# Kernel optimization log

Hardware: AMD Instinct MI355X
Metric: run time of the kernel (lower is better)

Reference implementation:

```python
import jax, jax.numpy as jnp
import numpy as np

N, E, G = 50000, 800000, 64
H, C = 4, 64
IN = 260
SPLITS = [7, 4, 6, 4, 8]  # types, levels, interchange, unrolling, tiling


def _glorot(k, shape):
    lim = (6.0 / (shape[0] + shape[-1])) ** 0.5
    return jax.random.uniform(k, shape, jnp.float32, -lim, lim)


def setup_inputs() -> dict:
    key = jax.random.key(0)
    ks = list(jax.random.split(key, 40))
    nk = lambda: ks.pop()
    x = jax.random.normal(nk(), (N, IN), jnp.float32)
    edge_index = jax.random.randint(nk(), (2, E), 0, N)
    batch = ((jnp.arange(N) * G) // N).astype(jnp.int32)  # sorted, every graph non-empty
    input_actions = jnp.stack([jax.random.randint(nk(), (G,), 0, s) for s in SPLITS], 0)
    p = dict(
        W1=_glorot(nk(), (IN, H * C)), a_s1=jax.random.normal(nk(), (H, C)) * 0.1,
        a_d1=jax.random.normal(nk(), (H, C)) * 0.1, b1=jnp.zeros((H * C,)),
        Wl1=_glorot(nk(), (H * C, C)), bl1=jnp.zeros((C,)),
        W2=_glorot(nk(), (C, H * C)), a_s2=jax.random.normal(nk(), (H, C)) * 0.1,
        a_d2=jax.random.normal(nk(), (H, C)) * 0.1, b2=jnp.zeros((H * C,)),
        Wl2=_glorot(nk(), (H * C, C)), bl2=jnp.zeros((C,)),
        Ws=_glorot(nk(), (4 * C, 2 * C)), bs=jnp.zeros((2 * C,)),
        Wsh=_glorot(nk(), (2 * C, C)), bsh=jnp.zeros((C,)),
        Wp1=_glorot(nk(), (C, C)), bp1=jnp.zeros((C,)),
        Wp2=_glorot(nk(), (C, C)), bp2=jnp.zeros((C,)),
        Wp3=_glorot(nk(), (C, sum(SPLITS))), bp3=jnp.zeros((sum(SPLITS),)),
        Wv1=_glorot(nk(), (C, C)), bv1=jnp.zeros((C,)),
        Wv2=_glorot(nk(), (C, C)), bv2=jnp.zeros((C,)),
        Wv3=_glorot(nk(), (C, 1)), bv3=jnp.zeros((1,)),
    )
    return dict(x=x, edge_index=edge_index, batch=batch, input_actions=input_actions, **p)


def gat_conv(x, W, a_src, a_dst, b, src, dst, n):
    h = (x @ W).reshape(n, H, C)                          # [N,H,C]
    es = (h * a_src).sum(-1)                              # [N,H]
    ed = (h * a_dst).sum(-1)
    e = jax.nn.leaky_relu(es[src] + ed[dst], 0.2)          # [Etot,H]
    m = jax.ops.segment_max(e, dst, n)
    ex = jnp.exp(e - m[dst])
    denom = jax.ops.segment_sum(ex, dst, n)
    alpha = ex / denom[dst]                                # edge softmax per dst node
    out = jax.ops.segment_sum(alpha[:, :, None] * h[src], dst, n)
    return out.reshape(n, H * C) + b


def pool(x, batch, g):
    cnt = jax.ops.segment_sum(jnp.ones((x.shape[0],), x.dtype), batch, g)
    mean = jax.ops.segment_sum(x, batch, g) / cnt[:, None]
    mx = jax.ops.segment_max(x, batch, g)
    return jnp.concatenate([mean, mx], -1)


def reference(x, edge_index, batch, input_actions, W1, a_s1, a_d1, b1, Wl1, bl1,
              W2, a_s2, a_d2, b2, Wl2, bl2, Ws, bs, Wsh, bsh,
              Wp1, bp1, Wp2, bp2, Wp3, bp3, Wv1, bv1, Wv2, bv2, Wv3, bv3):
    n = x.shape[0]
    loop = jnp.arange(n)
    src = jnp.concatenate([edge_index[0], loop])  # add self loops (PyG default)
    dst = jnp.concatenate([edge_index[1], loop])
    h = gat_conv(x, W1, a_s1, a_d1, b1, src, dst, n)
    h = jax.nn.selu(h @ Wl1 + bl1)
    x1 = pool(h, batch, G)
    h = gat_conv(h, W2, a_s2, a_d2, b2, src, dst, n)
    h = jax.nn.selu(h @ Wl2 + bl2)
    x2 = pool(h, batch, G)
    g = jnp.concatenate([x1, x2], -1) @ Ws + bs
    g = jax.nn.selu(g @ Wsh + bsh)
    hp = jax.nn.selu(g @ Wp1 + bp1)
    hp = jax.nn.selu(hp @ Wp2 + bp2)
    raw_logits = hp @ Wp3 + bp3
    hv = jax.nn.selu(g @ Wv1 + bv1)
    hv = jax.nn.selu(hv @ Wv2 + bv2)
    value = hv @ Wv3 + bv3                               # [G,1]
    parts = jnp.split(raw_logits, np.cumsum(SPLITS)[:-1].tolist(), axis=1)
    lps, ents = [], []
    for k, lg in enumerate(parts):
        logp = jax.nn.log_softmax(lg, -1)
        lps.append(jnp.take_along_axis(logp, input_actions[k][:, None], 1)[:, 0])
        ents.append(-(jnp.exp(logp) * logp).sum(-1))
    lp, en = jnp.stack(lps), jnp.stack(ents)              # [5,G]
    act = input_actions[0]
    bidx = jnp.arange(G)
    sel = jnp.clip(act - 1, 0, 4)
    lp_sel, en_sel = lp[sel, bidx], en[sel, bidx]
    zero = jnp.zeros_like(lp[0])
    final_lp = lp[0] + jnp.where(act < 3, lp[1], jnp.where(act < 5, lp_sel, jnp.where(act == 5, lp[1] + lp[4], zero)))
    final_en = en[0] + jnp.where(act < 3, en[1], jnp.where(act < 5, en_sel, jnp.where(act == 5, en[1] + en[4], zero)))
    return final_lp, final_en, value
```

## Files before the change

### kernel.cpp

```cpp
#include <hip/hip_runtime.h>
#include <math.h>

static constexpr int G_  = 64;
static constexpr int H_  = 4;
static constexpr int C_  = 64;
static constexpr int IN_ = 260;
static constexpr int HC_ = 256;
static constexpr int PAD_ = 64;
static constexpr int SLOTS_ = 16;

typedef short short8 __attribute__((ext_vector_type(8)));
typedef float f32x4 __attribute__((ext_vector_type(4)));

__device__ __forceinline__ float lrelu02(float x) { return x >= 0.f ? x : 0.2f * x; }
__device__ __forceinline__ float selu_f(float x) {
  const float sc = 1.0507009873554805f, al = 1.6732632423543772f;
  return x > 0.f ? sc * x : sc * al * expm1f(x);
}
__device__ __forceinline__ float bf2f(unsigned short u) {
  return __uint_as_float(((unsigned int)u) << 16);
}
__device__ __forceinline__ unsigned short f2bf(float f) {
  unsigned int u = __float_as_uint(f);
  u = (u + 0x7FFFu + ((u >> 16) & 1u)) >> 16;
  return (unsigned short)u;
}
__device__ __forceinline__ int lower_bound_i(const int* b, int n, int val) {
  int lo = 0, hi = n;
  while (lo < hi) {
    int mid = (lo + hi) >> 1;
    if (b[mid] < val) lo = mid + 1; else hi = mid;
  }
  return lo;
}

__global__ __launch_bounds__(256) void k_prep(const float* __restrict__ x, ushort4* __restrict__ xb,
                                              const float* __restrict__ W1, const float* __restrict__ W2,
                                              const float* __restrict__ Wl1, const float* __restrict__ Wl2,
                                              unsigned short* __restrict__ wout, int* __restrict__ cur,
                                              int* __restrict__ pcnt1, int* __restrict__ pcnt2,
                                              int n, int Mpad) {
  int idx = blockIdx.x * 256 + threadIdx.x;
  int castTotal = Mpad * 72;
  if (idx < castTotal) {
    int r = idx / 72, c4 = (idx - r * 72) * 4;
    ushort4 o = make_ushort4(0, 0, 0, 0);
    if (r < n && c4 < IN_) {
      float4 v = *(const float4*)&x[(size_t)r * IN_ + c4];
      o = make_ushort4(f2bf(v.x), f2bf(v.y), f2bf(v.z), f2bf(v.w));
    }
    xb[idx] = o;
    return;
  }
  idx -= castTotal;
  if (idx < 122880) {
    const float* W;
    int Kreal, KS, N, local;
    if (idx < 73728)       { W = W1;  Kreal = 260; KS = 9; N = 256; local = idx; }
    else if (idx < 90112)  { W = W2;  Kreal = 64;  KS = 2; N = 256; local = idx - 73728; }
    else if (idx < 106496) { W = Wl1; Kreal = 256; KS = 8; N = 64;  local = idx - 90112; }
    else                   { W = Wl2; Kreal = 256; KS = 8; N = 64;  local = idx - 106496; }
    int i = local & 7;
    int l = (local >> 3) & 63;
    int nb = (local >> 9) & 3;
    int ks = (local >> 11) % KS;
    int g = (local >> 11) / KS;
    int k = ks * 32 + ((l >> 4) << 3) + i;
    int n2 = g * 64 + nb * 16 + (l & 15);
    wout[idx] = (k < Kreal) ? f2bf(W[(size_t)k * N + n2]) : (unsigned short)0;
    return;
  }
  idx -= 122880;
  if (idx < n) { cur[idx] = 0; return; }
  idx -= n;
  if (idx < 1024) { pcnt1[idx] = 0; return; }
  idx -= 1024;
  if (idx < 1024) pcnt2[idx] = 0;
}

__global__ __launch_bounds__(256) void k_scatter(const int* __restrict__ src, const int* __restrict__ dst,
                                                 int* __restrict__ cur, unsigned short* __restrict__ csr, int E) {
  int e = blockIdx.x * 256 + threadIdx.x;
  if (e < E) {
    int d = dst[e];
    int pos = atomicAdd(&cur[d], 1);
    if (pos < PAD_) csr[(d << 6) + pos] = (unsigned short)src[e];
  }
}

template <int KS>
__global__ __launch_bounds__(256) void k_mgemm(const unsigned short* __restrict__ A,
                                               const unsigned short* __restrict__ Bp,
                                               unsigned short* __restrict__ C,
                                               int Kpad, int N) {
  extern __shared__ char smem[];
  unsigned short* lds = (unsigned short*)smem;
  int tid = threadIdx.x;
  int l = tid & 63;
  int w = tid >> 6;
  int g = blockIdx.y;
  {
    const float4* s = (const float4*)(Bp + (size_t)g * KS * 2048);
    float4* d = (float4*)lds;
    #pragma unroll
    for (int t = 0; t < KS; t++) d[t * 256 + tid] = s[t * 256 + tid];
  }
  __syncthreads();
  int rm = blockIdx.x * 256 + w * 64;
  const unsigned short* arow[4];
  #pragma unroll
  for (int mi = 0; mi < 4; mi++)
    arow[mi] = A + (size_t)(rm + mi * 16 + (l & 15)) * Kpad + ((l >> 4) << 3);
  f32x4 acc[4][4] = {};
  #pragma unroll
  for (int ks = 0; ks < KS; ks++) {
    short8 a[4], b[4];
    #pragma unroll
    for (int mi = 0; mi < 4; mi++) a[mi] = *(const short8*)(arow[mi] + ks * 32);
    #pragma unroll
    for (int nb = 0; nb < 4; nb++) b[nb] = *(const short8*)(lds + (((ks * 4 + nb) * 64) + l) * 8);
    #pragma unroll
    for (int mi = 0; mi < 4; mi++)
      #pragma unroll
      for (int nb = 0; nb < 4; nb++)
        acc[mi][nb] = __builtin_amdgcn_mfma_f32_16x16x32_bf16(a[mi], b[nb], acc[mi][nb], 0, 0, 0);
  }
  int cr = (l >> 4) * 4;
  int cc = l & 15;
  #pragma unroll
  for (int mi = 0; mi < 4; mi++) {
    #pragma unroll
    for (int nb = 0; nb < 4; nb++) {
      int col = g * 64 + nb * 16 + cc;
      int colp = (col & 63) * 4 + (col >> 6);
      #pragma unroll
      for (int r = 0; r < 4; r++)
        C[(size_t)(rm + mi * 16 + cr + r) * N + colp] = f2bf(acc[mi][nb][r]);
    }
  }
}

__global__ __launch_bounds__(256) void k_esedq(const unsigned short* __restrict__ h, const float* __restrict__ a_s,
                                               const float* __restrict__ a_d, float* __restrict__ esed,
                                               unsigned int* __restrict__ hq, float* __restrict__ scale, int n) {
  int lane = threadIdx.x & 63;
  int node = blockIdx.x * 4 + (threadIdx.x >> 6);
  if (node >= n) return;
  ushort4 u = *(const ushort4*)(h + (size_t)node * HC_ + lane * 4);
  float xv[4] = {bf2f(u.x), bf2f(u.y), bf2f(u.z), bf2f(u.w)};
  float s[H_], d[H_];
  float amax = 0.f;
  #pragma unroll
  for (int hh = 0; hh < H_; hh++) {
    s[hh] = xv[hh] * a_s[hh * C_ + lane];
    d[hh] = xv[hh] * a_d[hh * C_ + lane];
    amax = fmaxf(amax, fabsf(xv[hh]));
  }
  #pragma unroll
  for (int o2 = 32; o2 > 0; o2 >>= 1) {
    #pragma unroll
    for (int hh = 0; hh < H_; hh++) {
      s[hh] += __shfl_xor(s[hh], o2, 64);
      d[hh] += __shfl_xor(d[hh], o2, 64);
    }
    amax = fmaxf(amax, __shfl_xor(amax, o2, 64));
  }
  float sc = fmaxf(amax, 1e-6f) * (1.f / 127.f);
  float inv = 127.f / fmaxf(amax, 1e-6f);
  unsigned int q = 0;
  #pragma unroll
  for (int hh = 0; hh < H_; hh++) {
    int qi = __float2int_rn(xv[hh] * inv);
    qi = min(127, max(-127, qi)) + 128;
    q |= ((unsigned int)qi) << (8 * hh);
  }
  hq[(size_t)node * 64 + lane] = q;
  if (lane == 0) {
    scale[node] = sc;
    #pragma unroll
    for (int hh = 0; hh < H_; hh++) {
      esed[(size_t)node * 8 + hh] = s[hh];
      esed[(size_t)node * 8 + 4 + hh] = d[hh];
    }
  }
}

__global__ __launch_bounds__(256) void k_agg(const unsigned int* __restrict__ hq, const float* __restrict__ scale,
                                             const float* __restrict__ esed, const int* __restrict__ deg,
                                             const unsigned short* __restrict__ csr, const float* __restrict__ bias,
                                             unsigned short* __restrict__ out, int n) {
  __shared__ float4 wlds[4][64];
  __shared__ int slds[4][64];
  int lane = threadIdx.x & 63;
  int wv = threadIdx.x >> 6;
  int node = blockIdx.x * 4 + wv;
  if (node >= n) return;
  int nk = min(deg[node], PAD_);
  int e0 = node << 6;
  const float4 edv = ((const float4*)esed)[(size_t)node * 2 + 1];
  float acc0 = 0.f, acc1 = 0.f, acc2 = 0.f, acc3 = 0.f;
  float den[4] = {0.f, 0.f, 0.f, 0.f};
  float sw[4] = {0.f, 0.f, 0.f, 0.f};
  {
    float4 w4 = make_float4(0.f, 0.f, 0.f, 0.f);
    int sid = 0;
    if (lane < nk) {
      sid = csr[e0 + lane];
      float4 es = ((const float4*)esed)[(size_t)sid * 2];
      float sc = scale[sid];
      float w0 = __expf(lrelu02(es.x + edv.x));
      float w1 = __expf(lrelu02(es.y + edv.y));
      float w2 = __expf(lrelu02(es.z + edv.z));
      float w3 = __expf(lrelu02(es.w + edv.w));
      den[0] += w0; den[1] += w1; den[2] += w2; den[3] += w3;
      w4 = make_float4(w0 * sc, w1 * sc, w2 * sc, w3 * sc);
      sw[0] += w4.x; sw[1] += w4.y; sw[2] += w4.z; sw[3] += w4.w;
    }
    wlds[wv][lane] = w4;
    slds[wv][lane] = sid << 8;
  }
  const char* hqb = (const char*)hq + lane * 4;
#define AGG1(W, Q)                                        \
  acc0 = fmaf(W.x, (float)(Q & 0xffu), acc0);             \
  acc1 = fmaf(W.y, (float)((Q >> 8) & 0xffu), acc1);      \
  acc2 = fmaf(W.z, (float)((Q >> 16) & 0xffu), acc2);     \
  acc3 = fmaf(W.w, (float)(Q >> 24), acc3);
  int j = 0;
  for (; j + 4 <= nk; j += 4) {
    float4 wa = wlds[wv][j], wb = wlds[wv][j + 1], wc = wlds[wv][j + 2], wd = wlds[wv][j + 3];
    int oa = slds[wv][j], ob = slds[wv][j + 1], oc = slds[wv][j + 2], od = slds[wv][j + 3];
    unsigned int qa = *(const unsigned int*)(hqb + oa);
    unsigned int qb = *(const unsigned int*)(hqb + ob);
    unsigned int qc = *(const unsigned int*)(hqb + oc);
    unsigned int qd = *(const unsigned int*)(hqb + od);
    AGG1(wa, qa) AGG1(wb, qb) AGG1(wc, qc) AGG1(wd, qd)
  }
  for (; j < nk; j++) {
    float4 wj = wlds[wv][j];
    unsigned int q = *(const unsigned int*)(hqb + slds[wv][j]);
    AGG1(wj, q)
  }
#undef AGG1
  #pragma unroll
  for (int o2 = 32; o2 > 0; o2 >>= 1) {
    #pragma unroll
    for (int hh = 0; hh < 4; hh++) {
      den[hh] += __shfl_xor(den[hh], o2, 64);
      sw[hh] += __shfl_xor(sw[hh], o2, 64);
    }
  }
  const float4 esv = ((const float4*)esed)[(size_t)node * 2];
  float ssc = scale[node];
  unsigned int qs = hq[(size_t)node * 64 + lane];
  float es0 = __expf(lrelu02(esv.x + edv.x));
  float es1 = __expf(lrelu02(esv.y + edv.y));
  float es2 = __expf(lrelu02(esv.z + edv.z));
  float es3 = __expf(lrelu02(esv.w + edv.w));
  float w0 = es0 * ssc, w1 = es1 * ssc, w2 = es2 * ssc, w3 = es3 * ssc;
  acc0 = fmaf(w0, (float)(qs & 0xffu), acc0);
  acc1 = fmaf(w1, (float)((qs >> 8) & 0xffu), acc1);
  acc2 = fmaf(w2, (float)((qs >> 16) & 0xffu), acc2);
  acc3 = fmaf(w3, (float)(qs >> 24), acc3);
  den[0] += es0; den[1] += es1; den[2] += es2; den[3] += es3;
  sw[0] += w0; sw[1] += w1; sw[2] += w2; sw[3] += w3;
  float r0 = (acc0 - 128.f * sw[0]) / den[0];
  float r1 = (acc1 - 128.f * sw[1]) / den[1];
  float r2 = (acc2 - 128.f * sw[2]) / den[2];
  float r3 = (acc3 - 128.f * sw[3]) / den[3];
  out[(size_t)node * HC_ + 0 * C_ + lane] = f2bf(r0 + bias[0 * C_ + lane]);
  out[(size_t)node * HC_ + 1 * C_ + lane] = f2bf(r1 + bias[1 * C_ + lane]);
  out[(size_t)node * HC_ + 2 * C_ + lane] = f2bf(r2 + bias[2 * C_ + lane]);
  out[(size_t)node * HC_ + 3 * C_ + lane] = f2bf(r3 + bias[3 * C_ + lane]);
}

template <int PHASE2>
__global__ __launch_bounds__(256) void k_fuse(const unsigned short* __restrict__ gout,
                                              const unsigned short* __restrict__ Bl, const float* __restrict__ bl,
                                              const unsigned short* __restrict__ W2p,
                                              const float* __restrict__ as2, const float* __restrict__ ad2,
                                              float* __restrict__ esed, unsigned int* __restrict__ hq,
                                              float* __restrict__ scale,
                                              const int* __restrict__ batch,
                                              float* __restrict__ psum, float* __restrict__ pmax,
                                              int* __restrict__ pcnt, int n) {
  __shared__ unsigned short hs_lds[64 * 64];
  __shared__ float pA_s[4][64], pA_m[4][64], pB_s[4][64], pB_m[4][64];
  __shared__ int meta[4];
  int tid = threadIdx.x;
  int l = tid & 63;
  int w = tid >> 6;
  int bm = blockIdx.x * 64;
  {
    const unsigned short* arow = gout + (size_t)(bm + w * 16 + (l & 15)) * HC_ + ((l >> 4) << 3);
    f32x4 acc[4] = {};
    #pragma unroll
    for (int ks = 0; ks < 8; ks++) {
      short8 a = *(const short8*)(arow + ks * 32);
      #pragma unroll
      for (int nb = 0; nb < 4; nb++) {
        short8 b = *(const short8*)(Bl + (size_t)(ks * 2048 + nb * 512 + l * 8));
        acc[nb] = __builtin_amdgcn_mfma_f32_16x16x32_bf16(a, b, acc[nb], 0, 0, 0);
      }
    }
    #pragma unroll
    for (int nb = 0; nb < 4; nb++) {
      #pragma unroll
      for (int r = 0; r < 4; r++) {
        int row = w * 16 + (l >> 4) * 4 + r;
        int col = nb * 16 + (l & 15);
        float v = selu_f(acc[nb][r] + bl[col]);
        int chunk = (col >> 3) ^ (row & 7);
        hs_lds[row * 64 + chunk * 8 + (col & 7)] = f2bf(v);
      }
    }
  }
  __syncthreads();
  if (PHASE2) {
    f32x4 acc2[16] = {};
    #pragma unroll
    for (int ks2 = 0; ks2 < 2; ks2++) {
      int row = w * 16 + (l & 15);
      int chunk = (ks2 * 4 + (l >> 4)) ^ (row & 7);
      short8 a2 = *(const short8*)(hs_lds + row * 64 + chunk * 8);
      #pragma unroll
      for (int f = 0; f < 16; f++) {
        short8 b2 = *(const short8*)(W2p + (size_t)(((f >> 2) * 2 + ks2) * 2048 + (f & 3) * 512 + l * 8));
        acc2[f] = __builtin_amdgcn_mfma_f32_16x16x32_bf16(a2, b2, acc2[f], 0, 0, 0);
      }
    }
    float s_[4][4] = {}, d_[4][4] = {};
    float am[4] = {0.f, 0.f, 0.f, 0.f};
    #pragma unroll
    for (int f = 0; f < 16; f++) {
      int ch = (f >> 2) * 64 + (f & 3) * 16 + (l & 15);
      float asv = as2[ch], adv = ad2[ch];
      #pragma unroll
      for (int r = 0; r < 4; r++) {
        float v = acc2[f][r];
        s_[r][f >> 2] = fmaf(v, asv, s_[r][f >> 2]);
        d_[r][f >> 2] = fmaf(v, adv, d_[r][f >> 2]);
        am[r] = fmaxf(am[r], fabsf(v));
      }
    }
    #pragma unroll
    for (int off = 1; off < 16; off <<= 1) {
      #pragma unroll
      for (int r = 0; r < 4; r++) {
        #pragma unroll
        for (int g2 = 0; g2 < 4; g2++) {
          s_[r][g2] += __shfl_xor(s_[r][g2], off, 64);
          d_[r][g2] += __shfl_xor(d_[r][g2], off, 64);
        }
        am[r] = fmaxf(am[r], __shfl_xor(am[r], off, 64));
      }
    }
    #pragma unroll
    for (int r = 0; r < 4; r++) {
      int node = bm + w * 16 + (l >> 4) * 4 + r;
      if (node < n) {
        float amax = fmaxf(am[r], 1e-6f);
        float inv = 127.f / amax;
        #pragma unroll
        for (int nb = 0; nb < 4; nb++) {
          unsigned int q = 0;
          #pragma unroll
          for (int g2 = 0; g2 < 4; g2++) {
            int qi = __float2int_rn(acc2[g2 * 4 + nb][r] * inv);
            qi = min(127, max(-127, qi)) + 128;
            q |= ((unsigned int)qi) << (8 * g2);
          }
          hq[(size_t)node * 64 + nb * 16 + (l & 15)] = q;
        }
        int li = l & 15;
        if (li < 4) esed[(size_t)node * 8 + li] = s_[r][li];
        else if (li < 8) esed[(size_t)node * 8 + li] = d_[r][li - 4];
        else if (li == 8) scale[node] = amax * (1.f / 127.f);
      }
    }
  }
  if (tid == 0) {
    int gA = (bm < n) ? batch[bm] : -1;
    int valid = n - bm;
    valid = valid < 0 ? 0 : (valid > 64 ? 64 : valid);
    int split = valid, gB = -1;
    if (gA >= 0) {
      int lb = lower_bound_i(batch, n, gA + 1);
      split = lb - bm;
      if (split > valid) split = valid;
      if (split < valid) gB = batch[bm + split];
    }
    meta[0] = gA; meta[1] = split; meta[2] = gB; meta[3] = valid;
  }
  __syncthreads();
  int gA = meta[0], split = meta[1], gB = meta[2], valid = meta[3];
  if (gA < 0) return;
  {
    int ch = tid & 63, rs = tid >> 6;
    float sA = 0.f, mA = -INFINITY, sB = 0.f, mB = -INFINITY;
    #pragma unroll
    for (int k = 0; k < 16; k++) {
      int r = rs * 16 + k;
      if (r < valid) {
        int chunk = (ch >> 3) ^ (r & 7);
        float v = bf2f(hs_lds[r * 64 + chunk * 8 + (ch & 7)]);
        if (r < split) { sA += v; mA = fmaxf(mA, v); }
        else           { sB += v; mB = fmaxf(mB, v); }
      }
    }
    pA_s[rs][ch] = sA; pA_m[rs][ch] = mA;
    pB_s[rs][ch] = sB; pB_m[rs][ch] = mB;
  }
  __syncthreads();
  if (tid < 64) {
    float s = pA_s[0][tid] + pA_s[1][tid] + pA_s[2][tid] + pA_s[3][tid];
    float m = fmaxf(fmaxf(pA_m[0][tid], pA_m[1][tid]), fmaxf(pA_m[2][tid], pA_m[3][tid]));
    int slotA = (int)blockIdx.x - (lower_bound_i(batch, n, gA) >> 6);
    psum[((size_t)gA * SLOTS_ + slotA) * 64 + tid] = s;
    pmax[((size_t)gA * SLOTS_ + slotA) * 64 + tid] = m;
    if (tid == 0) pcnt[gA * SLOTS_ + slotA] = split;
  } else if (tid < 128 && gB >= 0) {
    int c2 = tid - 64;
    float s = pB_s[0][c2] + pB_s[1][c2] + pB_s[2][c2] + pB_s[3][c2];
    float m = fmaxf(fmaxf(pB_m[0][c2], pB_m[1][c2]), fmaxf(pB_m[2][c2], pB_m[3][c2]));
    psum[((size_t)gB * SLOTS_ + 0) * 64 + c2] = s;
    pmax[((size_t)gB * SLOTS_ + 0) * 64 + c2] = m;
    if (c2 == 0) pcnt[gB * SLOTS_] = valid - split;
  }
}

__global__ __launch_bounds__(128) void k_head(const float* __restrict__ psum1, const float* __restrict__ pmax1,
                                              const int* __restrict__ pcnt1,
                                              const float* __restrict__ psum2, const float* __restrict__ pmax2,
                                              const int* __restrict__ pcnt2, const int* __restrict__ ia,
                                              const float* __restrict__ Ws, const float* __restrict__ bs,
                                              const float* __restrict__ Wsh, const float* __restrict__ bsh,
                                              const float* __restrict__ Wp1, const float* __restrict__ bp1,
                                              const float* __restrict__ Wp2, const float* __restrict__ bp2,
                                              const float* __restrict__ Wp3, const float* __restrict__ bp3,
                                              const float* __restrict__ Wv1, const float* __restrict__ bv1,
                                              const float* __restrict__ Wv2, const float* __restrict__ bv2,
                                              const float* __restrict__ Wv3, const float* __restrict__ bv3,
                                              float* __restrict__ out) {
  int g = blockIdx.x;
  int t = threadIdx.x;
  __shared__ float row[256], t1[128], g2[64], ha[64], hb[64], ha2[64], hb2[64];
  __shared__ float logits[29], lps[5], ens[5];
  {
    const float* PS = (t < 64) ? psum1 : psum2;
    const float* PM = (t < 64) ? pmax1 : pmax2;
    const int* PC = (t < 64) ? pcnt1 : pcnt2;
    int c = t & 63;
    int o = (t < 64) ? 0 : 128;
    float sum = 0.f, mx = -INFINITY;
    int tot = 0;
    #pragma unroll
    for (int s = 0; s < SLOTS_; s++) {
      int c0 = PC[g * SLOTS_ + s];
      if (c0 > 0) {
        sum += PS[((size_t)g * SLOTS_ + s) * 64 + c];
        mx = fmaxf(mx, PM[((size_t)g * SLOTS_ + s) * 64 + c]);
        tot += c0;
      }
    }
    row[o + c] = sum / (float)tot;
    row[o + 64 + c] = mx;
  }
  __syncthreads();
  {
    float a = bs[t];
    for (int k = 0; k < 256; k++) a = fmaf(row[k], Ws[k * 128 + t], a);
    t1[t] = a;
  }
  __syncthreads();
  if (t < 64) {
    float a = bsh[t];
    for (int k = 0; k < 128; k++) a = fmaf(t1[k], Wsh[k * 64 + t], a);
    g2[t] = selu_f(a);
  }
  __syncthreads();
  if (t < 64) {
    float a = bp1[t];
    for (int k = 0; k < 64; k++) a = fmaf(g2[k], Wp1[k * 64 + t], a);
    ha[t] = selu_f(a);
  } else {
    int c = t - 64;
    float a = bv1[c];
    for (int k = 0; k < 64; k++) a = fmaf(g2[k], Wv1[k * 64 + c], a);
    hb[c] = selu_f(a);
  }
  __syncthreads();
  if (t < 64) {
    float a = bp2[t];
    for (int k = 0; k < 64; k++) a = fmaf(ha[k], Wp2[k * 64 + t], a);
    ha2[t] = selu_f(a);
  } else {
    int c = t - 64;
    float a = bv2[c];
    for (int k = 0; k < 64; k++) a = fmaf(hb[k], Wv2[k * 64 + c], a);
    hb2[c] = selu_f(a);
  }
  __syncthreads();
  if (t < 29) {
    float a = bp3[t];
    for (int k = 0; k < 64; k++) a = fmaf(ha2[k], Wp3[k * 29 + t], a);
    logits[t] = a;
  }
  if (t == 127) {
    float a = bv3[0];
    for (int k = 0; k < 64; k++) a = fmaf(hb2[k], Wv3[k], a);
    out[128 + g] = a;
  }
  __syncthreads();
  if (t < 5) {
    const int offs[6] = {0, 7, 11, 17, 21, 29};
    int o0 = offs[t], o1 = offs[t + 1];
    float m = -INFINITY;
    for (int j = o0; j < o1; j++) m = fmaxf(m, logits[j]);
    float Z = 0.f;
    for (int j = o0; j < o1; j++) Z += expf(logits[j] - m);
    float lz = logf(Z);
    int act = ia[t * G_ + g];
    lps[t] = logits[o0 + act] - m - lz;
    float ent = 0.f;
    for (int j = o0; j < o1; j++) {
      float lp_ = logits[j] - m - lz;
      ent -= expf(lp_) * lp_;
    }
    ens[t] = ent;
  }
  __syncthreads();
  if (t == 0) {
    int act = ia[g];
    int sel = min(max(act - 1, 0), 4);
    float flp, fen;
    if (act < 3) { flp = lps[1]; fen = ens[1]; }
    else if (act < 5) { flp = lps[sel]; fen = ens[sel]; }
    else if (act == 5) { flp = lps[1] + lps[4]; fen = ens[1] + ens[4]; }
    else { flp = 0.f; fen = 0.f; }
    out[g] = lps[0] + flp;
    out[G_ + g] = ens[0] + fen;
  }
}

extern "C" void kernel_launch(void* const* d_in, const int* in_sizes, int n_in,
                              void* d_out, int out_size, void* d_ws, size_t ws_size,
                              hipStream_t stream) {
  const float* x = (const float*)d_in[0];
  const int* ei = (const int*)d_in[1];
  const int* batch = (const int*)d_in[2];
  const int* ia = (const int*)d_in[3];
  const float* W1 = (const float*)d_in[4];
  const float* as1 = (const float*)d_in[5];
  const float* ad1 = (const float*)d_in[6];
  const float* b1 = (const float*)d_in[7];
  const float* Wl1 = (const float*)d_in[8];
  const float* bl1 = (const float*)d_in[9];
  const float* W2 = (const float*)d_in[10];
  const float* as2 = (const float*)d_in[11];
  const float* ad2 = (const float*)d_in[12];
  const float* b2 = (const float*)d_in[13];
  const float* Wl2 = (const float*)d_in[14];
  const float* bl2 = (const float*)d_in[15];
  const float* Ws = (const float*)d_in[16];
  const float* bs = (const float*)d_in[17];
  const float* Wsh = (const float*)d_in[18];
  const float* bsh = (const float*)d_in[19];
  const float* Wp1 = (const float*)d_in[20];
  const float* bp1 = (const float*)d_in[21];
  const float* Wp2 = (const float*)d_in[22];
  const float* bp2 = (const float*)d_in[23];
  const float* Wp3 = (const float*)d_in[24];
  const float* bp3 = (const float*)d_in[25];
  const float* Wv1 = (const float*)d_in[26];
  const float* bv1 = (const float*)d_in[27];
  const float* Wv2 = (const float*)d_in[28];
  const float* bv2 = (const float*)d_in[29];
  const float* Wv3 = (const float*)d_in[30];
  const float* bv3 = (const float*)d_in[31];
  float* out = (float*)d_out;

  const int n = in_sizes[0] / IN_;
  const int E = in_sizes[1] / 2;
  const int Mpad = ((n + 255) / 256) * 256;
  const int* src = ei;
  const int* dst = ei + E;

  char* w = (char*)d_ws;
  size_t cur_off = 0;
  auto alloc = [&](size_t bytes) -> char* {
    char* p = w + cur_off;
    cur_off = (cur_off + bytes + 255) & ~(size_t)255;
    return p;
  };
  int* cur = (int*)alloc((size_t)n * 4);
  int* pcnt1 = (int*)alloc((size_t)G_ * SLOTS_ * 4);
  int* pcnt2 = (int*)alloc((size_t)G_ * SLOTS_ * 4);
  unsigned short* csr = (unsigned short*)alloc((size_t)n * PAD_ * 2);
  unsigned short* xb = (unsigned short*)alloc((size_t)Mpad * 288 * 2);
  unsigned short* h = (unsigned short*)alloc((size_t)Mpad * HC_ * 2);
  float* esed = (float*)alloc((size_t)n * 8 * 4);
  float* scale = (float*)alloc((size_t)n * 4);
  unsigned int* hq = (unsigned int*)alloc((size_t)n * 256);
  unsigned short* gout = (unsigned short*)alloc((size_t)Mpad * HC_ * 2);
  unsigned short* Wp = (unsigned short*)alloc((size_t)122880 * 2);
  float* psum1 = (float*)alloc((size_t)G_ * SLOTS_ * 64 * 4);
  float* pmax1 = (float*)alloc((size_t)G_ * SLOTS_ * 64 * 4);
  float* psum2 = (float*)alloc((size_t)G_ * SLOTS_ * 64 * 4);
  float* pmax2 = (float*)alloc((size_t)G_ * SLOTS_ * 64 * 4);
  (void)ws_size;
  (void)n_in;
  (void)out_size;
  unsigned short* W1p = Wp;
  unsigned short* W2p = Wp + 73728;
  unsigned short* Wl1p = Wp + 90112;
  unsigned short* Wl2p = Wp + 106496;

  int prepTotal = Mpad * 72 + 122880 + n + 2048;
  k_prep<<<(prepTotal + 255) / 256, 256, 0, stream>>>(x, (ushort4*)xb, W1, W2, Wl1, Wl2, Wp,
                                                      cur, pcnt1, pcnt2, n, Mpad);
  int eb = (E + 255) / 256;
  k_scatter<<<eb, 256, 0, stream>>>(src, dst, cur, csr, E);

  int gx = Mpad / 256;
  int nwb = (n + 3) / 4;
  int fb = Mpad / 64;
  k_mgemm<9><<<dim3(gx, 4), 256, 9 * 4096, stream>>>(xb, W1p, h, 288, HC_);
  k_esedq<<<nwb, 256, 0, stream>>>(h, as1, ad1, esed, hq, scale, n);
  k_agg<<<nwb, 256, 0, stream>>>(hq, scale, esed, cur, csr, b1, gout, n);
  k_fuse<1><<<fb, 256, 0, stream>>>(gout, Wl1p, bl1, W2p, as2, ad2, esed, hq, scale,
                                    batch, psum1, pmax1, pcnt1, n);
  k_agg<<<nwb, 256, 0, stream>>>(hq, scale, esed, cur, csr, b2, gout, n);
  k_fuse<0><<<fb, 256, 0, stream>>>(gout, Wl2p, bl2, nullptr, nullptr, nullptr, nullptr, nullptr, nullptr,
                                    batch, psum2, pmax2, pcnt2, n);
  k_head<<<G_, 128, 0, stream>>>(psum1, pmax1, pcnt1, psum2, pmax2, pcnt2, ia, Ws, bs, Wsh, bsh,
                                 Wp1, bp1, Wp2, bp2, Wp3, bp3, Wv1, bv1, Wv2, bv2, Wv3, bv3, out);
}
```

Measured before the change: 298.9 us.

## Replace padded per-node edge buckets with exact CSR via count and prefix scan

Builds a compact CSR adjacency instead of the fixed 64-slot padded buckets. It counts in-degrees inside the prep kernel, runs a three-kernel block prefix scan to get offsets, then scatters source ids to exact positions. k_agg now reads offsets. This removes the truncation at 64 neighbours during the build and shrinks csr storage, but adds a memset, three small kernels and an extra atomic pass over all edges. Aggregation still caps each node's neighbour count at 64.

```diff
diff --git a/kernel.cpp b/kernel.cpp
--- a/kernel.cpp
+++ b/kernel.cpp
@@ -37,9 +37,10 @@
 __global__ __launch_bounds__(256) void k_prep(const float* __restrict__ x, ushort4* __restrict__ xb,
                                               const float* __restrict__ W1, const float* __restrict__ W2,
                                               const float* __restrict__ Wl1, const float* __restrict__ Wl2,
-                                              unsigned short* __restrict__ wout, int* __restrict__ cur,
+                                              unsigned short* __restrict__ wout,
                                               int* __restrict__ pcnt1, int* __restrict__ pcnt2,
-                                              int n, int Mpad) {
+                                              const int* __restrict__ dst, int* __restrict__ cnt,
+                                              int n, int Mpad, int E) {
   int idx = blockIdx.x * 256 + threadIdx.x;
   int castTotal = Mpad * 72;
   if (idx < castTotal) {
@@ -71,11 +72,76 @@
     return;
   }
   idx -= 122880;
-  if (idx < n) { cur[idx] = 0; return; }
-  idx -= n;
   if (idx < 1024) { pcnt1[idx] = 0; return; }
   idx -= 1024;
-  if (idx < 1024) pcnt2[idx] = 0;
+  if (idx < 1024) { pcnt2[idx] = 0; return; }
+  idx -= 1024;
+  if (idx < E) atomicAdd(&cnt[dst[idx]], 1);
+}
+
+__global__ __launch_bounds__(256) void k_bsum(const int* __restrict__ cnt, int* __restrict__ bsum, int n) {
+  int b = blockIdx.x, tid = threadIdx.x;
+  int i0 = b * 1024 + tid * 4;
+  int s = 0;
+  #pragma unroll
+  for (int j = 0; j < 4; j++)
+    if (i0 + j < n) s += cnt[i0 + j];
+  #pragma unroll
+  for (int o = 32; o > 0; o >>= 1) s += __shfl_xor(s, o, 64);
+  __shared__ int ws_[4];
+  if ((tid & 63) == 0) ws_[tid >> 6] = s;
+  __syncthreads();
+  if (tid == 0) bsum[b] = ws_[0] + ws_[1] + ws_[2] + ws_[3];
+}
+
+__global__ __launch_bounds__(64) void k_bscan(int* __restrict__ bsum, int nb, int* __restrict__ off,
+                                              int n, int total) {
+  int lane = threadIdx.x;
+  int carry = 0;
+  for (int base = 0; base < nb; base += 64) {
+    int v = (base + lane < nb) ? bsum[base + lane] : 0;
+    int sc = v;
+    #pragma unroll
+    for (int s = 1; s < 64; s <<= 1) {
+      int t = __shfl_up(sc, s, 64);
+      if (lane >= s) sc += t;
+    }
+    if (base + lane < nb) bsum[base + lane] = carry + sc - v;
+    carry += __shfl(sc, 63, 64);
+  }
+  if (lane == 0) off[n] = total;
+}
+
+__global__ __launch_bounds__(256) void k_boff(const int* __restrict__ cnt, const int* __restrict__ bpre,
+                                              int* __restrict__ off, int* __restrict__ cur, int n) {
+  int b = blockIdx.x, tid = threadIdx.x;
+  int lane = tid & 63, w = tid >> 6;
+  int i0 = b * 1024 + tid * 4;
+  int v[4];
+  #pragma unroll
+  for (int j = 0; j < 4; j++) v[j] = (i0 + j < n) ? cnt[i0 + j] : 0;
+  int ts = v[0] + v[1] + v[2] + v[3];
+  int sc = ts;
+  #pragma unroll
+  for (int s = 1; s < 64; s <<= 1) {
+    int t = __shfl_up(sc, s, 64);
+    if (lane >= s) sc += t;
+  }
+  __shared__ int wsum[4], wpre[4];
+  if (lane == 63) wsum[w] = sc;
+  __syncthreads();
+  if (tid == 0) {
+    int a = 0;
+    #pragma unroll
+    for (int k = 0; k < 4; k++) { wpre[k] = a; a += wsum[k]; }
+  }
+  __syncthreads();
+  int excl = bpre[b] + wpre[w] + sc - ts;
+  #pragma unroll
+  for (int j = 0; j < 4; j++) {
+    if (i0 + j < n) { off[i0 + j] = excl; cur[i0 + j] = excl; }
+    excl += v[j];
+  }
 }
 
 __global__ __launch_bounds__(256) void k_scatter(const int* __restrict__ src, const int* __restrict__ dst,
@@ -84,7 +150,7 @@
   if (e < E) {
     int d = dst[e];
     int pos = atomicAdd(&cur[d], 1);
-    if (pos < PAD_) csr[(d << 6) + pos] = (unsigned short)src[e];
+    csr[pos] = (unsigned short)src[e];
   }
 }
 
@@ -186,7 +252,7 @@
 }
 
 __global__ __launch_bounds__(256) void k_agg(const unsigned int* __restrict__ hq, const float* __restrict__ scale,
-                                             const float* __restrict__ esed, const int* __restrict__ deg,
+                                             const float* __restrict__ esed, const int* __restrict__ off,
                                              const unsigned short* __restrict__ csr, const float* __restrict__ bias,
                                              unsigned short* __restrict__ out, int n) {
   __shared__ float4 wlds[4][64];
@@ -195,8 +261,8 @@
   int wv = threadIdx.x >> 6;
   int node = blockIdx.x * 4 + wv;
   if (node >= n) return;
-  int nk = min(deg[node], PAD_);
-  int e0 = node << 6;
+  int e0 = off[node];
+  int nk = min(off[node + 1] - e0, PAD_);
   const float4 edv = ((const float4*)esed)[(size_t)node * 2 + 1];
   float acc0 = 0.f, acc1 = 0.f, acc2 = 0.f, acc3 = 0.f;
   float den[4] = {0.f, 0.f, 0.f, 0.f};
@@ -343,15 +409,15 @@
       }
     }
     #pragma unroll
-    for (int off = 1; off < 16; off <<= 1) {
+    for (int off2 = 1; off2 < 16; off2 <<= 1) {
       #pragma unroll
       for (int r = 0; r < 4; r++) {
         #pragma unroll
         for (int g2 = 0; g2 < 4; g2++) {
-          s_[r][g2] += __shfl_xor(s_[r][g2], off, 64);
-          d_[r][g2] += __shfl_xor(d_[r][g2], off, 64);
+          s_[r][g2] += __shfl_xor(s_[r][g2], off2, 64);
+          d_[r][g2] += __shfl_xor(d_[r][g2], off2, 64);
         }
-        am[r] = fmaxf(am[r], __shfl_xor(am[r], off, 64));
+        am[r] = fmaxf(am[r], __shfl_xor(am[r], off2, 64));
       }
     }
     #pragma unroll
@@ -582,6 +648,7 @@
   const int n = in_sizes[0] / IN_;
   const int E = in_sizes[1] / 2;
   const int Mpad = ((n + 255) / 256) * 256;
+  const int nb = (n + 1023) / 1024;
   const int* src = ei;
   const int* dst = ei + E;
 
@@ -592,10 +659,13 @@
     cur_off = (cur_off + bytes + 255) & ~(size_t)255;
     return p;
   };
+  int* cnt = (int*)alloc((size_t)n * 4);
+  int* off = (int*)alloc((size_t)(n + 1) * 4);
   int* cur = (int*)alloc((size_t)n * 4);
+  int* bsum = (int*)alloc((size_t)(nb + 1) * 4);
   int* pcnt1 = (int*)alloc((size_t)G_ * SLOTS_ * 4);
   int* pcnt2 = (int*)alloc((size_t)G_ * SLOTS_ * 4);
-  unsigned short* csr = (unsigned short*)alloc((size_t)n * PAD_ * 2);
+  unsigned short* csr = (unsigned short*)alloc((size_t)E * 2);
   unsigned short* xb = (unsigned short*)alloc((size_t)Mpad * 288 * 2);
   unsigned short* h = (unsigned short*)alloc((size_t)Mpad * HC_ * 2);
   float* esed = (float*)alloc((size_t)n * 8 * 4);
@@ -615,9 +685,13 @@
   unsigned short* Wl1p = Wp + 90112;
   unsigned short* Wl2p = Wp + 106496;
 
-  int prepTotal = Mpad * 72 + 122880 + n + 2048;
+  hipMemsetAsync(cnt, 0, (size_t)n * 4, stream);
+  int prepTotal = Mpad * 72 + 122880 + 2048 + E;
   k_prep<<<(prepTotal + 255) / 256, 256, 0, stream>>>(x, (ushort4*)xb, W1, W2, Wl1, Wl2, Wp,
-                                                      cur, pcnt1, pcnt2, n, Mpad);
+                                                      pcnt1, pcnt2, dst, cnt, n, Mpad, E);
+  k_bsum<<<nb, 256, 0, stream>>>(cnt, bsum, n);
+  k_bscan<<<1, 64, 0, stream>>>(bsum, nb, off, n, E);
+  k_boff<<<nb, 256, 0, stream>>>(cnt, bsum, off, cur, n);
   int eb = (E + 255) / 256;
   k_scatter<<<eb, 256, 0, stream>>>(src, dst, cur, csr, E);
 
@@ -626,10 +700,10 @@
   int fb = Mpad / 64;
   k_mgemm<9><<<dim3(gx, 4), 256, 9 * 4096, stream>>>(xb, W1p, h, 288, HC_);
   k_esedq<<<nwb, 256, 0, stream>>>(h, as1, ad1, esed, hq, scale, n);
-  k_agg<<<nwb, 256, 0, stream>>>(hq, scale, esed, cur, csr, b1, gout, n);
+  k_agg<<<nwb, 256, 0, stream>>>(hq, scale, esed, off, csr, b1, gout, n);
   k_fuse<1><<<fb, 256, 0, stream>>>(gout, Wl1p, bl1, W2p, as2, ad2, esed, hq, scale,
                                     batch, psum1, pmax1, pcnt1, n);
-  k_agg<<<nwb, 256, 0, stream>>>(hq, scale, esed, cur, csr, b2, gout, n);
+  k_agg<<<nwb, 256, 0, stream>>>(hq, scale, esed, off, csr, b2, gout, n);
   k_fuse<0><<<fb, 256, 0, stream>>>(gout, Wl2p, bl2, nullptr, nullptr, nullptr, nullptr, nullptr, nullptr,
                                     batch, psum2, pmax2, pcnt2, n);
   k_head<<<G_, 128, 0, stream>>>(psum1, pmax1, pcnt1, psum2, pmax2, pcnt2, ia, Ws, bs, Wsh, bsh,
```

Result: slower. 338.9 us (+13.4%).

## Fuse layer-1 GEMM with attention-score and int8 quantization epilogue

Applied to the files above, without the earlier changes.

Replaces the separate bf16 GEMM (which wrote h to global) and the k_esedq pass with one kernel that computes the x@W1 tile via MFMA and directly produces attention scores, per-node scale and quantized features. This removes the h round-trip through global memory and one launch. W1 fragments are now read straight from global/cache instead of staged in LDS, and each block does only 64 rows, which may raise weight traffic. Separately, the CSR neighbour list changes from 16-bit to 32-bit ints written with atomicExch, which fixes truncation for node ids above 65535 but doubles CSR bytes.

```diff
diff --git a/kernel.cpp b/kernel.cpp
--- a/kernel.cpp
+++ b/kernel.cpp
@@ -79,115 +79,89 @@
 }
 
 __global__ __launch_bounds__(256) void k_scatter(const int* __restrict__ src, const int* __restrict__ dst,
-                                                 int* __restrict__ cur, unsigned short* __restrict__ csr, int E) {
+                                                 int* __restrict__ cur, int* __restrict__ csr, int E) {
   int e = blockIdx.x * 256 + threadIdx.x;
   if (e < E) {
     int d = dst[e];
     int pos = atomicAdd(&cur[d], 1);
-    if (pos < PAD_) csr[(d << 6) + pos] = (unsigned short)src[e];
-  }
-}
-
-template <int KS>
-__global__ __launch_bounds__(256) void k_mgemm(const unsigned short* __restrict__ A,
-                                               const unsigned short* __restrict__ Bp,
-                                               unsigned short* __restrict__ C,
-                                               int Kpad, int N) {
-  extern __shared__ char smem[];
-  unsigned short* lds = (unsigned short*)smem;
+    if (pos < PAD_) atomicExch(&csr[(d << 6) + pos], src[e]);
+  }
+}
+
+__global__ __launch_bounds__(256) void k_l1(const unsigned short* __restrict__ xb,
+                                            const unsigned short* __restrict__ W1p,
+                                            const float* __restrict__ as1, const float* __restrict__ ad1,
+                                            float* __restrict__ esed, unsigned int* __restrict__ hq,
+                                            float* __restrict__ scale, int n) {
   int tid = threadIdx.x;
   int l = tid & 63;
   int w = tid >> 6;
-  int g = blockIdx.y;
-  {
-    const float4* s = (const float4*)(Bp + (size_t)g * KS * 2048);
-    float4* d = (float4*)lds;
-    #pragma unroll
-    for (int t = 0; t < KS; t++) d[t * 256 + tid] = s[t * 256 + tid];
-  }
-  __syncthreads();
-  int rm = blockIdx.x * 256 + w * 64;
-  const unsigned short* arow[4];
+  int bm = blockIdx.x * 64;
+  const unsigned short* arow = xb + (size_t)(bm + w * 16 + (l & 15)) * 288 + ((l >> 4) << 3);
+  f32x4 acc2[16] = {};
   #pragma unroll
-  for (int mi = 0; mi < 4; mi++)
-    arow[mi] = A + (size_t)(rm + mi * 16 + (l & 15)) * Kpad + ((l >> 4) << 3);
-  f32x4 acc[4][4] = {};
+  for (int ks = 0; ks < 9; ks++) {
+    short8 a = *(const short8*)(arow + ks * 32);
+    #pragma unroll
+    for (int f = 0; f < 16; f++) {
+      short8 b = *(const short8*)(W1p + (size_t)(((f >> 2) * 9 + ks) * 2048 + (f & 3) * 512 + l * 8));
+      acc2[f] = __builtin_amdgcn_mfma_f32_16x16x32_bf16(a, b, acc2[f], 0, 0, 0);
+    }
+  }
+  float s_[4][4] = {}, d_[4][4] = {};
+  float am[4] = {0.f, 0.f, 0.f, 0.f};
   #pragma unroll
-  for (int ks = 0; ks < KS; ks++) {
-    short8 a[4], b[4];
-    #pragma unroll
-    for (int mi = 0; mi < 4; mi++) a[mi] = *(const short8*)(arow[mi] + ks * 32);
-    #pragma unroll
-    for (int nb = 0; nb < 4; nb++) b[nb] = *(const short8*)(lds + (((ks * 4 + nb) * 64) + l) * 8);
-    #pragma unroll
-    for (int mi = 0; mi < 4; mi++)
+  for (int f = 0; f < 16; f++) {
+    int ch = (f >> 2) * 64 + (f & 3) * 16 + (l & 15);
+    float asv = as1[ch], adv = ad1[ch];
+    #pragma unroll
+    for (int r = 0; r < 4; r++) {
+      float v = acc2[f][r];
+      s_[r][f >> 2] = fmaf(v, asv, s_[r][f >> 2]);
+      d_[r][f >> 2] = fmaf(v, adv, d_[r][f >> 2]);
+      am[r] = fmaxf(am[r], fabsf(v));
+    }
+  }
+  #pragma unroll
+  for (int off2 = 1; off2 < 16; off2 <<= 1) {
+    #pragma unroll
+    for (int r = 0; r < 4; r++) {
       #pragma unroll
-      for (int nb = 0; nb < 4; nb++)
-        acc[mi][nb] = __builtin_amdgcn_mfma_f32_16x16x32_bf16(a[mi], b[nb], acc[mi][nb], 0, 0, 0);
-  }
-  int cr = (l >> 4) * 4;
-  int cc = l & 15;
+      for (int g2 = 0; g2 < 4; g2++) {
+        s_[r][g2] += __shfl_xor(s_[r][g2], off2, 64);
+        d_[r][g2] += __shfl_xor(d_[r][g2], off2, 64);
+      }
+      am[r] = fmaxf(am[r], __shfl_xor(am[r], off2, 64));
+    }
+  }
   #pragma unroll
-  for (int mi = 0; mi < 4; mi++) {
-    #pragma unroll
-    for (int nb = 0; nb < 4; nb++) {
-      int col = g * 64 + nb * 16 + cc;
-      int colp = (col & 63) * 4 + (col >> 6);
+  for (int r = 0; r < 4; r++) {
+    int node = bm + w * 16 + (l >> 4) * 4 + r;
+    if (node < n) {
+      float amax = fmaxf(am[r], 1e-6f);
+      float inv = 127.f / amax;
       #pragma unroll
-      for (int r = 0; r < 4; r++)
-        C[(size_t)(rm + mi * 16 + cr + r) * N + colp] = f2bf(acc[mi][nb][r]);
-    }
-  }
-}
-
-__global__ __launch_bounds__(256) void k_esedq(const unsigned short* __restrict__ h, const float* __restrict__ a_s,
-                                               const float* __restrict__ a_d, float* __restrict__ esed,
-                                               unsigned int* __restrict__ hq, float* __restrict__ scale, int n) {
-  int lane = threadIdx.x & 63;
-  int node = blockIdx.x * 4 + (threadIdx.x >> 6);
-  if (node >= n) return;
-  ushort4 u = *(const ushort4*)(h + (size_t)node * HC_ + lane * 4);
-  float xv[4] = {bf2f(u.x), bf2f(u.y), bf2f(u.z), bf2f(u.w)};
-  float s[H_], d[H_];
-  float amax = 0.f;
-  #pragma unroll
-  for (int hh = 0; hh < H_; hh++) {
-    s[hh] = xv[hh] * a_s[hh * C_ + lane];
-    d[hh] = xv[hh] * a_d[hh * C_ + lane];
-    amax = fmaxf(amax, fabsf(xv[hh]));
-  }
-  #pragma unroll
-  for (int o2 = 32; o2 > 0; o2 >>= 1) {
-    #pragma unroll
-    for (int hh = 0; hh < H_; hh++) {
-      s[hh] += __shfl_xor(s[hh], o2, 64);
-      d[hh] += __shfl_xor(d[hh], o2, 64);
-    }
-    amax = fmaxf(amax, __shfl_xor(amax, o2, 64));
-  }
-  float sc = fmaxf(amax, 1e-6f) * (1.f / 127.f);
-  float inv = 127.f / fmaxf(amax, 1e-6f);
-  unsigned int q = 0;
-  #pragma unroll
-  for (int hh = 0; hh < H_; hh++) {
-    int qi = __float2int_rn(xv[hh] * inv);
-    qi = min(127, max(-127, qi)) + 128;
-    q |= ((unsigned int)qi) << (8 * hh);
-  }
-  hq[(size_t)node * 64 + lane] = q;
-  if (lane == 0) {
-    scale[node] = sc;
-    #pragma unroll
-    for (int hh = 0; hh < H_; hh++) {
-      esed[(size_t)node * 8 + hh] = s[hh];
-      esed[(size_t)node * 8 + 4 + hh] = d[hh];
+      for (int nb = 0; nb < 4; nb++) {
+        unsigned int q = 0;
+        #pragma unroll
+        for (int g2 = 0; g2 < 4; g2++) {
+          int qi = __float2int_rn(acc2[g2 * 4 + nb][r] * inv);
+          qi = min(127, max(-127, qi)) + 128;
+          q |= ((unsigned int)qi) << (8 * g2);
+        }
+        hq[(size_t)node * 64 + nb * 16 + (l & 15)] = q;
+      }
+      int li = l & 15;
+      if (li < 4) esed[(size_t)node * 8 + li] = s_[r][li];
+      else if (li < 8) esed[(size_t)node * 8 + li] = d_[r][li - 4];
+      else if (li == 8) scale[node] = amax * (1.f / 127.f);
     }
   }
 }
 
 __global__ __launch_bounds__(256) void k_agg(const unsigned int* __restrict__ hq, const float* __restrict__ scale,
                                              const float* __restrict__ esed, const int* __restrict__ deg,
-                                             const unsigned short* __restrict__ csr, const float* __restrict__ bias,
+                                             const int* __restrict__ csr, const float* __restrict__ bias,
                                              unsigned short* __restrict__ out, int n) {
   __shared__ float4 wlds[4][64];
   __shared__ int slds[4][64];
@@ -343,15 +317,15 @@
       }
     }
     #pragma unroll
-    for (int off = 1; off < 16; off <<= 1) {
+    for (int off2 = 1; off2 < 16; off2 <<= 1) {
       #pragma unroll
       for (int r = 0; r < 4; r++) {
         #pragma unroll
         for (int g2 = 0; g2 < 4; g2++) {
-          s_[r][g2] += __shfl_xor(s_[r][g2], off, 64);
-          d_[r][g2] += __shfl_xor(d_[r][g2], off, 64);
+          s_[r][g2] += __shfl_xor(s_[r][g2], off2, 64);
+          d_[r][g2] += __shfl_xor(d_[r][g2], off2, 64);
         }
-        am[r] = fmaxf(am[r], __shfl_xor(am[r], off, 64));
+        am[r] = fmaxf(am[r], __shfl_xor(am[r], off2, 64));
       }
     }
     #pragma unroll
@@ -595,9 +569,8 @@
   int* cur = (int*)alloc((size_t)n * 4);
   int* pcnt1 = (int*)alloc((size_t)G_ * SLOTS_ * 4);
   int* pcnt2 = (int*)alloc((size_t)G_ * SLOTS_ * 4);
-  unsigned short* csr = (unsigned short*)alloc((size_t)n * PAD_ * 2);
+  int* csr = (int*)alloc((size_t)n * PAD_ * 4);
   unsigned short* xb = (unsigned short*)alloc((size_t)Mpad * 288 * 2);
-  unsigned short* h = (unsigned short*)alloc((size_t)Mpad * HC_ * 2);
   float* esed = (float*)alloc((size_t)n * 8 * 4);
   float* scale = (float*)alloc((size_t)n * 4);
   unsigned int* hq = (unsigned int*)alloc((size_t)n * 256);
@@ -621,11 +594,9 @@
   int eb = (E + 255) / 256;
   k_scatter<<<eb, 256, 0, stream>>>(src, dst, cur, csr, E);
 
-  int gx = Mpad / 256;
   int nwb = (n + 3) / 4;
   int fb = Mpad / 64;
-  k_mgemm<9><<<dim3(gx, 4), 256, 9 * 4096, stream>>>(xb, W1p, h, 288, HC_);
-  k_esedq<<<nwb, 256, 0, stream>>>(h, as1, ad1, esed, hq, scale, n);
+  k_l1<<<fb, 256, 0, stream>>>(xb, W1p, as1, ad1, esed, hq, scale, n);
   k_agg<<<nwb, 256, 0, stream>>>(hq, scale, esed, cur, csr, b1, gout, n);
   k_fuse<1><<<fb, 256, 0, stream>>>(gout, Wl1p, bl1, W2p, as2, ad2, esed, hq, scale,
                                     batch, psum1, pmax1, pcnt1, n);
```

Result: faster. 282.4 us (-5.5%).
